# Optimization experiments

Measured on AMD Instinct MI355X. Metric: run time of the kernel, lower is better.

## Reference

```python
import jax, jax.numpy as jnp
import numpy as np

IN_C, HID1, HID2 = 128, 256, 32
N_NODES = 50000
N_EDGES = 1600000
N_LABEL = 200000


def setup_inputs() -> dict:
    key = jax.random.key(0)
    ks = jax.random.split(key, 8)
    x = jax.random.normal(ks[0], (N_NODES, IN_C), dtype=jnp.float32)
    edge_index = jax.random.randint(ks[1], (2, N_EDGES), 0, N_NODES, dtype=jnp.int64)
    edge_label_index = jax.random.randint(ks[2], (2, N_LABEL), 0, N_NODES, dtype=jnp.int64)
    # GCNConv params (glorot-ish scale), bias zeros as default init
    W1 = jax.random.normal(ks[3], (IN_C, HID1), dtype=jnp.float32) * (1.0 / np.sqrt(IN_C))
    b1 = jnp.zeros((HID1,), dtype=jnp.float32)
    W2 = jax.random.normal(ks[4], (HID1, HID2), dtype=jnp.float32) * (1.0 / np.sqrt(HID1))
    b2 = jnp.zeros((HID2,), dtype=jnp.float32)
    return {"x": x, "edge_index": edge_index, "edge_label_index": edge_label_index,
            "W1": W1, "b1": b1, "W2": W2, "b2": b2}


def _gcn_conv(x, W, b, src, dst, n_nodes):
    # GCNConv: h = x @ W; add self-loops; symmetric deg^{-1/2} normalization; scatter-add; + bias
    h = x @ W  # [N, out]
    loop = jnp.arange(n_nodes, dtype=src.dtype)
    s = jnp.concatenate([src, loop])
    d = jnp.concatenate([dst, loop])
    deg = jax.ops.segment_sum(jnp.ones_like(d, dtype=h.dtype), d, num_segments=n_nodes)
    dinv = jnp.where(deg > 0, jax.lax.rsqrt(deg), 0.0)
    coef = dinv[s] * dinv[d]  # [E+N]
    msg = h[s] * coef[:, None]  # irregular gather, [E+N, out]
    agg = jax.ops.segment_sum(msg, d, num_segments=n_nodes)
    return agg + b


def reference(x, edge_index, edge_label_index, W1, b1, W2, b2):
    n = x.shape[0]
    src, dst = edge_index[0], edge_index[1]
    # encode (dropout p=0, use_bn=False -> identity)
    h = _gcn_conv(x, W1, b1, src, dst, n)
    h = jax.nn.relu(h)
    z = _gcn_conv(h, W2, b2, src, dst, n)
    # decode: edge-wise dot product
    return (z[edge_label_index[0]] * z[edge_label_index[1]]).sum(axis=-1)
```

## Files before the change

### kernel.cpp

```cpp
#include <hip/hip_runtime.h>
#include <hip/hip_fp16.h>

#define IN_C 128
#define H1   256
#define H2   32
#define BWL  6
#define NBMAX 1024
#define BCAP 2560
#define CSRCAP 4096

typedef _Float16 half8 __attribute__((ext_vector_type(8)));
typedef _Float16 half4 __attribute__((ext_vector_type(4)));
typedef _Float16 h2    __attribute__((ext_vector_type(2)));
typedef float f32x4 __attribute__((ext_vector_type(4)));
typedef unsigned short us8 __attribute__((ext_vector_type(8)));

__global__ __launch_bounds__(256) void k_scatter(const int* __restrict__ src, const int* __restrict__ dst,
                                                 int* bucket_cursor, unsigned int* __restrict__ binned,
                                                 const float* __restrict__ W1, const float* __restrict__ W2,
                                                 _Float16* __restrict__ W1s, _Float16* __restrict__ W2s,
                                                 int e, int nb) {
  __shared__ int hist[NBMAX];
  __shared__ int wbase[NBMAX];
  int t = threadIdx.x;
  for (int u = t; u < nb; u += 256) hist[u] = 0;
  __syncthreads();
  int base = blockIdx.x * 8192;
  int s_[32], d_[32], r_[32];
  #pragma unroll
  for (int j = 0; j < 32; j++) {
    int i = base + j * 256 + t;
    if (i < e) {
      s_[j] = src[i]; d_[j] = dst[i];
      r_[j] = atomicAdd(&hist[d_[j] >> BWL], 1);
    } else d_[j] = -1;
  }
  __syncthreads();
  for (int u = t; u < nb; u += 256) {
    int c = hist[u];
    wbase[u] = (c > 0) ? (u * BCAP + atomicAdd(&bucket_cursor[u], c)) : 0;
  }
  __syncthreads();
  #pragma unroll
  for (int j = 0; j < 32; j++) {
    if (d_[j] >= 0)
      binned[wbase[d_[j] >> BWL] + r_[j]] = ((unsigned)(d_[j] & 63) << 16) | (unsigned)s_[j];
  }
  int i = blockIdx.x * 256 + t;
  if (i < 128 * 256) {
    int d = i >> 3, j = i & 7;
    int mrow = d & 15, quad = (d >> 4) & 3, ks = (d >> 6) & 3, nt = d >> 8;
    W1s[i] = (_Float16)W1[(ks * 32 + quad * 8 + j) * 256 + nt * 16 + mrow];
  }
  if (i < 32 * 256) {
    int d = i >> 3, j = i & 7;
    int mrow = d & 15, quad = (d >> 4) & 3, ks = (d >> 6) & 7, nt = d >> 9;
    W2s[i] = (_Float16)W2[(ks * 32 + quad * 8 + j) * 32 + nt * 16 + mrow];
  }
}

__global__ __launch_bounds__(256) void k_fill2(const unsigned int* __restrict__ binned,
                                               const int* __restrict__ bucket_cursor,
                                               unsigned short* __restrict__ csr16,
                                               int* __restrict__ offsets, int* __restrict__ ecnt,
                                               float* __restrict__ dinv,
                                               const float4* __restrict__ x4, half4* __restrict__ xh4,
                                               int n, int nb) {
  __shared__ int cnt[64], pre[64], loc[64];
  __shared__ float sdinv[64];
  int b = blockIdx.x;
  int t = threadIdx.x;
  if (t < 64) cnt[t] = 0;
  {
    us8 dv;
    #pragma unroll
    for (int q = 0; q < 8; q++) dv[q] = (unsigned short)n;
    us8* cp = (us8*)(csr16 + (size_t)b * CSRCAP);
    for (int i = t; i < CSRCAP / 8; i += 256) cp[i] = dv;
  }
  __syncthreads();
  int start = b * BCAP, end = start + bucket_cursor[b];
  int startc = b * CSRCAP;
  int node0 = b << BWL;
  unsigned int recs[10]; int ranks[10];
  int ne = 0;
  for (int i = start + t; i < end; i += 256) {
    unsigned int rec = binned[i];
    int li = (int)(rec >> 16);
    ranks[ne] = atomicAdd(&cnt[li], 1);
    recs[ne++] = rec;
  }
  __syncthreads();
  int v = (t < 64) ? cnt[t] : 0;
  int vp = (v + 31) & ~31;
  if (t < 64) pre[t] = vp;
  __syncthreads();
  for (int off = 1; off < 64; off <<= 1) {
    int x = (t >= off && t < 64) ? pre[t - off] : 0;
    __syncthreads();
    if (t < 64) pre[t] += x;
    __syncthreads();
  }
  if (t < 64) {
    int excl = pre[t] - vp;
    loc[t] = excl;
    float dn = rsqrtf((float)(v + 1));
    sdinv[t] = dn;
    int node = node0 + t;
    if (node < n) {
      offsets[node] = startc + excl;
      ecnt[node] = v;
      dinv[node] = dn;
    }
  }
  __syncthreads();
  for (int k = 0; k < ne; k++) {
    int li = (int)(recs[k] >> 16);
    csr16[startc + loc[li] + ranks[k]] = (unsigned short)(recs[k] & 0xFFFFu);
  }
  for (int q = t; q < 64 * 32; q += 256) {
    int nd = node0 + (q >> 5);
    if (nd < n) {
      int c4 = q & 31;
      float4 vv = x4[(size_t)nd * 32 + c4];
      float dn = sdinv[q >> 5];
      half4 o;
      o[0] = (_Float16)(vv.x * dn); o[1] = (_Float16)(vv.y * dn);
      o[2] = (_Float16)(vv.z * dn); o[3] = (_Float16)(vv.w * dn);
      xh4[(size_t)nd * 32 + c4] = o;
    }
  }
}

__global__ __launch_bounds__(256) void k_agg1(const half8* __restrict__ xh8, const float* __restrict__ dinv,
                                              const int* __restrict__ ecnt, const int* __restrict__ offsets,
                                              const unsigned short* __restrict__ csr16,
                                              half8* __restrict__ aggh8, int n, int nblk) {
  int pass = blockIdx.x / nblk;
  int blk  = blockIdx.x - pass * nblk;
  int node = blk * 4 + (threadIdx.x >> 6);
  int lane = threadIdx.x & 63;
  int g  = lane >> 2;
  int c8 = (lane & 3) + pass * 4;
  if (node >= n) return;
  float acc[8];
  #pragma unroll
  for (int k = 0; k < 8; k++) acc[k] = 0.f;
  int start = offsets[node];
  int cnt = ecnt[node];
  int units = ((cnt + 31) & ~31) >> 5;
  int s0 = csr16[start + g], s1 = csr16[start + 16 + g];
  for (int u = 0; u < units; u++) {
    int t0 = 0, t1 = 0;
    if (u + 1 < units) {
      int nb = start + ((u + 1) << 5) + g;
      t0 = csr16[nb]; t1 = csr16[nb + 16];
    }
    half8 v0 = xh8[(size_t)s0 * 16 + c8];
    half8 v1 = xh8[(size_t)s1 * 16 + c8];
    half8 sA = v0 + v1;
    #pragma unroll
    for (int k = 0; k < 8; k++) acc[k] += (float)sA[k];
    s0 = t0; s1 = t1;
  }
  #pragma unroll
  for (int k = 0; k < 8; k++) {
    acc[k] += __shfl_xor(acc[k], 4, 64);
    acc[k] += __shfl_xor(acc[k], 8, 64);
    acc[k] += __shfl_xor(acc[k], 16, 64);
    acc[k] += __shfl_xor(acc[k], 32, 64);
  }
  if (g == 0) {
    half8 selfv = xh8[(size_t)node * 16 + c8];
    float dn = dinv[node];
    half8 o;
    #pragma unroll
    for (int k = 0; k < 8; k++) o[k] = (_Float16)((acc[k] + (float)selfv[k]) * dn);
    aggh8[(size_t)node * 16 + c8] = o;
  }
}

__global__ __launch_bounds__(256) void k_gemm12(const _Float16* __restrict__ aggh,
                                                const _Float16* __restrict__ W1s, const float* __restrict__ b1,
                                                const _Float16* __restrict__ W2s, const float* __restrict__ dinv,
                                                _Float16* __restrict__ h2h, int n) {
  __shared__ _Float16 wlds[128 * 256];
  int wid = threadIdx.x >> 6, lane = threadIdx.x & 63;
  int quad = lane >> 4, mrow = lane & 15;
  int mbase = blockIdx.x * 64 + wid * 16;
  int node = mbase + mrow; if (node >= n) node = n - 1;
  {
    half8* wl8 = (half8*)wlds;
    const half8* wg8 = (const half8*)W1s;
    for (int i = threadIdx.x; i < 4096; i += 256) wl8[i] = wg8[i];
  }
  __syncthreads();
  const half8* A = (const half8*)aggh;
  const half8* BL = (const half8*)wlds;
  f32x4 acc[16];
  #pragma unroll
  for (int t = 0; t < 16; t++) acc[t] = (f32x4){0.f, 0.f, 0.f, 0.f};
  half8 a_cur = A[(size_t)node * 16 + quad];
  #pragma unroll
  for (int ks = 0; ks < 4; ks++) {
    half8 a = a_cur;
    if (ks < 3) a_cur = A[(size_t)node * 16 + (ks + 1) * 4 + quad];
    #pragma unroll
    for (int nt = 0; nt < 16; nt++) {
      half8 b = BL[(nt * 4 + ks) * 64 + lane];
      acc[nt] = __builtin_amdgcn_mfma_f32_16x16x32_f16(a, b, acc[nt], 0, 0, 0);
    }
  }
  __syncthreads();
  _Float16* h1t = wlds;
  #pragma unroll
  for (int nt = 0; nt < 16; nt++) {
    int c = nt * 16 + mrow;
    float bias = b1[c];
    #pragma unroll
    for (int r = 0; r < 4; r++)
      h1t[(wid * 16 + quad * 4 + r) * 264 + c] = (_Float16)fmaxf(acc[nt][r] + bias, 0.f);
  }
  __syncthreads();
  const half8* B2 = (const half8*)W2s;
  f32x4 acc2[2];
  acc2[0] = (f32x4){0.f, 0.f, 0.f, 0.f};
  acc2[1] = (f32x4){0.f, 0.f, 0.f, 0.f};
  #pragma unroll
  for (int ks = 0; ks < 8; ks++) {
    const half8* arow = (const half8*)&h1t[(wid * 16 + mrow) * 264 + ks * 32 + quad * 8];
    half8 a = *arow;
    half8 b0 = B2[(0 * 8 + ks) * 64 + lane];
    half8 b1f = B2[(1 * 8 + ks) * 64 + lane];
    acc2[0] = __builtin_amdgcn_mfma_f32_16x16x32_f16(a, b0,  acc2[0], 0, 0, 0);
    acc2[1] = __builtin_amdgcn_mfma_f32_16x16x32_f16(a, b1f, acc2[1], 0, 0, 0);
  }
  #pragma unroll
  for (int nt = 0; nt < 2; nt++) {
    int c = nt * 16 + mrow;
    #pragma unroll
    for (int r = 0; r < 4; r++) {
      int m = mbase + quad * 4 + r;
      if (m < n) h2h[(size_t)m * H2 + c] = (_Float16)(acc2[nt][r] * dinv[m]);
    }
  }
}

__global__ __launch_bounds__(256) void k_agg2(const half4* __restrict__ h2h4, const float* __restrict__ dinv,
                                              const int* __restrict__ ecnt, const int* __restrict__ offsets,
                                              const unsigned short* __restrict__ csr16,
                                              const float* __restrict__ b2, half4* __restrict__ zh4, int n) {
  int node = blockIdx.x * 4 + (threadIdx.x >> 6);
  int lane = threadIdx.x & 63;
  int g = lane >> 3;
  int c4 = lane & 7;
  if (node >= n) return;
  float acc[4];
  #pragma unroll
  for (int k = 0; k < 4; k++) acc[k] = 0.f;
  int start = offsets[node];
  int cnt = ecnt[node];
  int units = ((cnt + 31) & ~31) >> 5;
  int s0 = csr16[start + g],      s1 = csr16[start + 8 + g];
  int s2 = csr16[start + 16 + g], s3 = csr16[start + 24 + g];
  for (int u = 0; u < units; u++) {
    int t0 = 0, t1 = 0, t2 = 0, t3 = 0;
    if (u + 1 < units) {
      int nb = start + ((u + 1) << 5) + g;
      t0 = csr16[nb]; t1 = csr16[nb + 8]; t2 = csr16[nb + 16]; t3 = csr16[nb + 24];
    }
    half4 vA = h2h4[(size_t)s0 * 8 + c4], vB = h2h4[(size_t)s1 * 8 + c4];
    half4 vC = h2h4[(size_t)s2 * 8 + c4], vD = h2h4[(size_t)s3 * 8 + c4];
    half4 sS = (vA + vB) + (vC + vD);
    #pragma unroll
    for (int k = 0; k < 4; k++) acc[k] += (float)sS[k];
    s0 = t0; s1 = t1; s2 = t2; s3 = t3;
  }
  #pragma unroll
  for (int k = 0; k < 4; k++) {
    acc[k] += __shfl_xor(acc[k], 8, 64);
    acc[k] += __shfl_xor(acc[k], 16, 64);
    acc[k] += __shfl_xor(acc[k], 32, 64);
  }
  if (g == 0) {
    half4 selfv = h2h4[(size_t)node * 8 + c4];
    float dn = dinv[node];
    half4 o;
    #pragma unroll
    for (int k = 0; k < 4; k++) o[k] = (_Float16)((acc[k] + (float)selfv[k]) * dn + b2[c4 * 4 + k]);
    zh4[(size_t)node * 8 + c4] = o;
  }
}

__global__ __launch_bounds__(512) void k_decode(const half4* __restrict__ zh4, const int* __restrict__ eli,
                                                float* __restrict__ out, int L) {
  int p = blockIdx.x * 64 + (threadIdx.x >> 3);
  int c4 = threadIdx.x & 7;
  if (p >= L) return;
  int a = eli[p], b = eli[L + p];
  half4 za = zh4[(size_t)a * 8 + c4];
  half4 zb = zh4[(size_t)b * 8 + c4];
  h2 zal = {za[0], za[1]}, zah = {za[2], za[3]};
  h2 zbl = {zb[0], zb[1]}, zbh = {zb[2], zb[3]};
  float v = __builtin_amdgcn_fdot2(zal, zbl, __builtin_amdgcn_fdot2(zah, zbh, 0.f, false), false);
  #pragma unroll
  for (int off = 4; off >= 1; off >>= 1) v += __shfl_xor(v, off, 64);
  if (c4 == 0) out[p] = v;
}

extern "C" void kernel_launch(void* const* d_in, const int* in_sizes, int n_in,
                              void* d_out, int out_size, void* d_ws, size_t ws_size,
                              hipStream_t stream) {
  const float* x   = (const float*)d_in[0];
  const int*   ei  = (const int*)d_in[1];
  const int*   eli = (const int*)d_in[2];
  const float* W1  = (const float*)d_in[3];
  const float* b1  = (const float*)d_in[4];
  const float* W2  = (const float*)d_in[5];
  const float* b2  = (const float*)d_in[6];
  float* out = (float*)d_out;

  const int N = in_sizes[0] / IN_C;
  const int E = in_sizes[1] / 2;
  const int L = in_sizes[2] / 2;
  const int* e_src = ei;
  const int* e_dst = ei + E;
  const int NB = (N + 63) >> BWL;

  char* p = (char*)d_ws;
  auto carve = [&](size_t bytes) -> void* {
    void* r = (void*)p;
    p += (bytes + 255) & ~(size_t)255;
    return r;
  };
  int*   ecnt      = (int*)  carve((size_t)N * 4);
  float* dinv      = (float*)carve((size_t)N * 4);
  int*   offsets   = (int*)  carve((size_t)N * 4);
  int*   bcursor   = (int*)  carve((NBMAX + 1) * 4);
  _Float16* W1s    = (_Float16*)carve(256 * 128 * 2);
  _Float16* W2s    = (_Float16*)carve(32 * 256 * 2);
  unsigned short* csr16 = (unsigned short*)carve(((size_t)NB * CSRCAP + 64) * 2);
  unsigned int* binned  = (unsigned int*)carve((size_t)NB * BCAP * 4);
  h2*    xh        = (h2*)   carve((size_t)(N + 1) * IN_C * 2);
  h2*    aggh      = (h2*)   carve(((size_t)N + 64) * IN_C * 2);
  _Float16* h2h    = (_Float16*)carve(((size_t)N + 64) * H2 * 2);
  half4* zh4       = (half4*)carve((size_t)N * H2 * 2);
  half4* h2h4 = (half4*)h2h;

  const int B = 256;
  const int nblk = (N + 3) / 4;
  hipMemsetAsync(bcursor, 0, (size_t)(NBMAX + 1) * 4, stream);
  hipMemsetAsync((char*)xh + (size_t)N * IN_C * 2, 0, IN_C * 2, stream);
  hipMemsetAsync((char*)h2h + (size_t)N * H2 * 2, 0, H2 * 2, stream);
  k_scatter<<<(E + 8191) / 8192, B, 0, stream>>>(e_src, e_dst, bcursor, binned,
                                                 W1, W2, W1s, W2s, E, NB);
  k_fill2<<<NB, B, 0, stream>>>(binned, bcursor, csr16, offsets, ecnt, dinv,
                                (const float4*)x, (half4*)xh, N, NB);
  k_agg1<<<4 * nblk, B, 0, stream>>>((const half8*)xh, dinv, ecnt, offsets, csr16, (half8*)aggh, N, nblk);
  k_gemm12<<<(N + 63) / 64, B, 0, stream>>>((const _Float16*)aggh, W1s, b1, W2s, dinv, h2h, N);
  k_agg2<<<(N + 3) / 4, B, 0, stream>>>(h2h4, dinv, ecnt, offsets, csr16, b2, zh4, N);
  k_decode<<<(L + 63) / 64, 512, 0, stream>>>(zh4, eli, out, L);
}
```

Measured before the change: 265.2 us.

## Restructure edge aggregation to vector-load neighbor indices and widen per-wave gathers

After: 222.8 us. 1.19x faster.

```diff
diff --git a/kernel.cpp b/kernel.cpp
--- a/kernel.cpp
+++ b/kernel.cpp
@@ -14,6 +14,7 @@
 typedef _Float16 h2    __attribute__((ext_vector_type(2)));
 typedef float f32x4 __attribute__((ext_vector_type(4)));
 typedef unsigned short us8 __attribute__((ext_vector_type(8)));
+typedef unsigned short us4 __attribute__((ext_vector_type(4)));
 
 __global__ __launch_bounds__(256) void k_scatter(const int* __restrict__ src, const int* __restrict__ dst,
                                                  int* bucket_cursor, unsigned int* __restrict__ binned,
@@ -135,13 +136,11 @@
 __global__ __launch_bounds__(256) void k_agg1(const half8* __restrict__ xh8, const float* __restrict__ dinv,
                                               const int* __restrict__ ecnt, const int* __restrict__ offsets,
                                               const unsigned short* __restrict__ csr16,
-                                              half8* __restrict__ aggh8, int n, int nblk) {
-  int pass = blockIdx.x / nblk;
-  int blk  = blockIdx.x - pass * nblk;
-  int node = blk * 4 + (threadIdx.x >> 6);
+                                              half8* __restrict__ aggh8, int n) {
+  int node = blockIdx.x * 4 + (threadIdx.x >> 6);
   int lane = threadIdx.x & 63;
-  int g  = lane >> 2;
-  int c8 = (lane & 3) + pass * 4;
+  int g = lane >> 4;
+  int c8 = lane & 15;
   if (node >= n) return;
   float acc[8];
   #pragma unroll
@@ -149,24 +148,21 @@
   int start = offsets[node];
   int cnt = ecnt[node];
   int units = ((cnt + 31) & ~31) >> 5;
-  int s0 = csr16[start + g], s1 = csr16[start + 16 + g];
+  us8 idx = *(const us8*)(csr16 + start + g * 8);
   for (int u = 0; u < units; u++) {
-    int t0 = 0, t1 = 0;
-    if (u + 1 < units) {
-      int nb = start + ((u + 1) << 5) + g;
-      t0 = csr16[nb]; t1 = csr16[nb + 16];
-    }
-    half8 v0 = xh8[(size_t)s0 * 16 + c8];
-    half8 v1 = xh8[(size_t)s1 * 16 + c8];
-    half8 sA = v0 + v1;
-    #pragma unroll
-    for (int k = 0; k < 8; k++) acc[k] += (float)sA[k];
-    s0 = t0; s1 = t1;
+    half8 v0 = xh8[(size_t)idx[0] * 16 + c8], v1 = xh8[(size_t)idx[1] * 16 + c8];
+    half8 v2 = xh8[(size_t)idx[2] * 16 + c8], v3 = xh8[(size_t)idx[3] * 16 + c8];
+    half8 v4 = xh8[(size_t)idx[4] * 16 + c8], v5 = xh8[(size_t)idx[5] * 16 + c8];
+    half8 v6 = xh8[(size_t)idx[6] * 16 + c8], v7 = xh8[(size_t)idx[7] * 16 + c8];
+    us8 nidx = *(const us8*)(csr16 + start + ((u + 1) << 5) + g * 8);
+    asm volatile("" :: "v"(v0), "v"(v1), "v"(v2), "v"(v3), "v"(v4), "v"(v5), "v"(v6), "v"(v7));
+    half8 s = (((v0 + v1) + (v2 + v3)) + ((v4 + v5) + (v6 + v7)));
+    #pragma unroll
+    for (int k = 0; k < 8; k++) acc[k] += (float)s[k];
+    idx = nidx;
   }
   #pragma unroll
   for (int k = 0; k < 8; k++) {
-    acc[k] += __shfl_xor(acc[k], 4, 64);
-    acc[k] += __shfl_xor(acc[k], 8, 64);
     acc[k] += __shfl_xor(acc[k], 16, 64);
     acc[k] += __shfl_xor(acc[k], 32, 64);
   }
@@ -261,20 +257,16 @@
   int start = offsets[node];
   int cnt = ecnt[node];
   int units = ((cnt + 31) & ~31) >> 5;
-  int s0 = csr16[start + g],      s1 = csr16[start + 8 + g];
-  int s2 = csr16[start + 16 + g], s3 = csr16[start + 24 + g];
+  us4 idx = *(const us4*)(csr16 + start + g * 4);
   for (int u = 0; u < units; u++) {
-    int t0 = 0, t1 = 0, t2 = 0, t3 = 0;
-    if (u + 1 < units) {
-      int nb = start + ((u + 1) << 5) + g;
-      t0 = csr16[nb]; t1 = csr16[nb + 8]; t2 = csr16[nb + 16]; t3 = csr16[nb + 24];
-    }
-    half4 vA = h2h4[(size_t)s0 * 8 + c4], vB = h2h4[(size_t)s1 * 8 + c4];
-    half4 vC = h2h4[(size_t)s2 * 8 + c4], vD = h2h4[(size_t)s3 * 8 + c4];
+    half4 vA = h2h4[(size_t)idx[0] * 8 + c4], vB = h2h4[(size_t)idx[1] * 8 + c4];
+    half4 vC = h2h4[(size_t)idx[2] * 8 + c4], vD = h2h4[(size_t)idx[3] * 8 + c4];
+    us4 nidx = *(const us4*)(csr16 + start + ((u + 1) << 5) + g * 4);
+    asm volatile("" :: "v"(vA), "v"(vB), "v"(vC), "v"(vD));
     half4 sS = (vA + vB) + (vC + vD);
     #pragma unroll
     for (int k = 0; k < 4; k++) acc[k] += (float)sS[k];
-    s0 = t0; s1 = t1; s2 = t2; s3 = t3;
+    idx = nidx;
   }
   #pragma unroll
   for (int k = 0; k < 4; k++) {
@@ -348,7 +340,6 @@
   half4* h2h4 = (half4*)h2h;
 
   const int B = 256;
-  const int nblk = (N + 3) / 4;
   hipMemsetAsync(bcursor, 0, (size_t)(NBMAX + 1) * 4, stream);
   hipMemsetAsync((char*)xh + (size_t)N * IN_C * 2, 0, IN_C * 2, stream);
   hipMemsetAsync((char*)h2h + (size_t)N * H2 * 2, 0, H2 * 2, stream);
@@ -356,7 +347,7 @@
                                                  W1, W2, W1s, W2s, E, NB);
   k_fill2<<<NB, B, 0, stream>>>(binned, bcursor, csr16, offsets, ecnt, dinv,
                                 (const float4*)x, (half4*)xh, N, NB);
-  k_agg1<<<4 * nblk, B, 0, stream>>>((const half8*)xh, dinv, ecnt, offsets, csr16, (half8*)aggh, N, nblk);
+  k_agg1<<<(N + 3) / 4, B, 0, stream>>>((const half8*)xh, dinv, ecnt, offsets, csr16, (half8*)aggh, N);
   k_gemm12<<<(N + 63) / 64, B, 0, stream>>>((const _Float16*)aggh, W1s, b1, W2s, dinv, h2h, N);
   k_agg2<<<(N + 3) / 4, B, 0, stream>>>(h2h4, dinv, ecnt, offsets, csr16, b2, zh4, N);
   k_decode<<<(L + 63) / 64, 512, 0, stream>>>(zh4, eli, out, L);
```
